# Kernel optimization log

Measured on AMD Instinct MI355X. Metric: run time of the kernel, lower is better.

## Reference

```python
import jax, jax.numpy as jnp
import numpy as np

RES0 = 128
SCALES = [1, 2, 4, 8]
OUT_DIM = 32
PLANES = [(0, 1), (0, 2), (1, 2)]  # itertools.combinations(range(3), 2)


def _bilinear(grid, cx, cy):
    """grid: [C,H,W]; cx maps to W, cy maps to H; coords in [-1,1].
    Matches F.grid_sample(mode='bilinear', align_corners=True, padding_mode='border')."""
    C, H, W = grid.shape
    x = jnp.clip((cx + 1.0) * 0.5 * (W - 1), 0.0, W - 1)
    y = jnp.clip((cy + 1.0) * 0.5 * (H - 1), 0.0, H - 1)
    x0 = jnp.floor(x)
    y0 = jnp.floor(y)
    wx = (x - x0)[:, None]  # [N,1]
    wy = (y - y0)[:, None]
    x0i = x0.astype(jnp.int32)
    y0i = y0.astype(jnp.int32)
    x1i = jnp.minimum(x0i + 1, W - 1)
    y1i = jnp.minimum(y0i + 1, H - 1)
    g00 = grid[:, y0i, x0i].T  # [N,C]
    g01 = grid[:, y0i, x1i].T
    g10 = grid[:, y1i, x0i].T
    g11 = grid[:, y1i, x1i].T
    top = g00 * (1.0 - wx) + g01 * wx
    bot = g10 * (1.0 - wx) + g11 * wx
    return top * (1.0 - wy) + bot * wy  # [N,C]


def _interpolate_ms_features(x, ms_grids):
    feats = []
    for scale_grids in ms_grids:  # fixed 4 scales
        interp_space = 1.0
        for ci, (a, b) in enumerate(PLANES):  # fixed 3 planes
            interp_space = interp_space * _bilinear(scale_grids[ci], x[:, a], x[:, b])
        feats.append(interp_space)
    return jnp.concatenate(feats, axis=-1)  # [N, 4*OUT_DIM]


def _mlp(f, w0, w1, w2):
    h = jax.nn.relu(f @ w0)
    h = jax.nn.relu(h @ w1)
    return h @ w2  # [N,1], linear output (tcnn, bias-free)


def setup_inputs() -> dict:
    key = jax.random.key(0)
    ks = jax.random.split(key, 16)
    N = 1_000_000
    inp = {"x": jax.random.uniform(ks[0], (N, 3), jnp.float32, -1.0, 1.0)}
    i = 1
    for s, mult in enumerate(SCALES):
        R = RES0 * mult
        for p in range(3):
            # nn.init.uniform_(a=0.1, b=0.5)
            inp[f"g{s}p{p}"] = jax.random.uniform(ks[i], (OUT_DIM, R, R), jnp.float32, 0.1, 0.5)
            i += 1
    F = OUT_DIM * len(SCALES)
    inp["w0"] = jax.random.normal(ks[13], (F, 64), jnp.float32) / np.sqrt(F).astype(np.float32)
    inp["w1"] = jax.random.normal(ks[14], (64, 64), jnp.float32) / 8.0
    inp["w2"] = jax.random.normal(ks[15], (64, 1), jnp.float32) / 8.0
    return inp


def reference(x, g0p0, g0p1, g0p2, g1p0, g1p1, g1p2, g2p0, g2p1, g2p2,
              g3p0, g3p1, g3p2, w0, w1, w2):
    ms_grids = [(g0p0, g0p1, g0p2), (g1p0, g1p1, g1p2),
                (g2p0, g2p1, g2p2), (g3p0, g3p1, g3p2)]
    features = _interpolate_ms_features(x, ms_grids)
    return _mlp(features, w0, w1, w2)
```

## Files before the change

### kernel.cpp

```cpp
#include <hip/hip_runtime.h>
#include <cstddef>


typedef unsigned short ushort_t;
typedef unsigned int uint_t;
typedef __bf16 bf16x8 __attribute__((ext_vector_type(8)));
typedef float f32x4 __attribute__((ext_vector_type(4)));

#define NBUCKET 32768

struct KParams {
  const float* x;
  const void* g[12];
  const float* w0;
  const float* w1;
  const float* w2;
  const ushort_t* w0T;
  const ushort_t* w1T;
  const float* xs;
  const int* sidx;
  float* out;
  int N;
};

struct TP3 {
  const float* src[3];
  ushort_t* dst[3];
  int RR;
};

__device__ __forceinline__ ushort_t f32_to_bf16_rne(float f) {
  uint_t u = __float_as_uint(f);
  u = (u + 0x7FFFu + ((u >> 16) & 1u)) >> 16;
  return (ushort_t)u;
}

__global__ __launch_bounds__(256) void transpose3(TP3 tp) {
  const float* __restrict__ in = tp.src[blockIdx.y];
  ushort_t* __restrict__ out = tp.dst[blockIdx.y];
  const int RR = tp.RR;
  __shared__ float tile[32][65];
  const int p0 = blockIdx.x * 64;
  {
    const int tp_ = threadIdx.x & 63;
    const int tc = threadIdx.x >> 6;
#pragma unroll
    for (int cc = 0; cc < 8; ++cc) {
      const int c = cc * 4 + tc;
      tile[c][tp_] = in[(size_t)c * RR + p0 + tp_];
    }
  }
  __syncthreads();
  {
    const int c2 = threadIdx.x & 15;
    const int tq = threadIdx.x >> 4;
    uint_t* o32 = (uint_t*)out;
#pragma unroll
    for (int pp = 0; pp < 4; ++pp) {
      const int pos = pp * 16 + tq;
      const uint_t lo = f32_to_bf16_rne(tile[2 * c2 + 0][pos]);
      const uint_t hi = f32_to_bf16_rne(tile[2 * c2 + 1][pos]);
      o32[(size_t)(p0 + pos) * 16 + c2] = lo | (hi << 16);
    }
  }
}

__global__ __launch_bounds__(256) void prep_weights(
    const float* __restrict__ w0, const float* __restrict__ w1,
    ushort_t* __restrict__ w0T, ushort_t* __restrict__ w1T) {
  const int t = threadIdx.x;
  for (int i = t; i < 128 * 64; i += 256) {
    const int k = i >> 6, n = i & 63;
    w0T[n * 128 + k] = f32_to_bf16_rne(w0[i]);
  }
  for (int i = t; i < 64 * 64; i += 256) {
    const int k = i >> 6, n = i & 63;
    w1T[n * 64 + k] = f32_to_bf16_rne(w1[i]);
  }
}

__device__ __forceinline__ uint_t spread5(uint_t v) {
  return (v & 1u) | ((v & 2u) << 2) | ((v & 4u) << 4) | ((v & 8u) << 6) |
         ((v & 16u) << 8);
}
__device__ __forceinline__ uint_t morton_key(const float* __restrict__ x,
                                             int i) {
  const float a = x[3 * i + 0];
  const float b = x[3 * i + 1];
  const float c = x[3 * i + 2];
  const uint_t ua = (uint_t)fminf(fmaxf((a + 1.0f) * 16.0f, 0.0f), 31.0f);
  const uint_t ub = (uint_t)fminf(fmaxf((b + 1.0f) * 16.0f, 0.0f), 31.0f);
  const uint_t uc = (uint_t)fminf(fmaxf((c + 1.0f) * 16.0f, 0.0f), 31.0f);
  return spread5(ua) | (spread5(ub) << 1) | (spread5(uc) << 2);
}

__global__ __launch_bounds__(256) void sort_hist(const float* __restrict__ x,
                                                 uint_t* __restrict__ cnt,
                                                 int N) {
  const int i = blockIdx.x * 256 + threadIdx.x;
  if (i < N) atomicAdd(&cnt[morton_key(x, i)], 1u);
}

__global__ __launch_bounds__(1024) void sort_scan(uint_t* __restrict__ cnt) {
  __shared__ uint_t s[1024];
  const int t = threadIdx.x;
  const int base = t * 32;
  uint_t p = 0;
#pragma unroll
  for (int e = 0; e < 32; ++e) p += cnt[base + e];
  s[t] = p;
  __syncthreads();
  for (int off = 1; off < 1024; off <<= 1) {
    uint_t v = 0;
    if (t >= off) v = s[t - off];
    __syncthreads();
    s[t] += v;
    __syncthreads();
  }
  uint_t running = s[t] - p;
#pragma unroll
  for (int e = 0; e < 32; ++e) {
    const uint_t old = cnt[base + e];
    cnt[base + e] = running;
    running += old;
  }
}

__global__ __launch_bounds__(256) void sort_scatter(
    const float* __restrict__ x, uint_t* __restrict__ cnt,
    int* __restrict__ sidx, float* __restrict__ xs, int N) {
  const int i = blockIdx.x * 256 + threadIdx.x;
  if (i >= N) return;
  const uint_t key = morton_key(x, i);
  const uint_t pos = atomicAdd(&cnt[key], 1u);
  sidx[pos] = i;
  xs[3 * pos + 0] = x[3 * i + 0];
  xs[3 * pos + 1] = x[3 * i + 1];
  xs[3 * pos + 2] = x[3 * i + 2];
}

template <bool SORTED>
__global__ __launch_bounds__(512, 8) void kplanes_fused_mfma(KParams P) {
  __shared__ float arena[10240];
  int* ci = (int*)arena;
  float* cf = arena;
  uint_t* feat32 = (uint_t*)(arena + 6144);
  float* px = arena + 6144;

  const int t = threadIdx.x;

  int bid = blockIdx.x;
  if (SORTED) {
    const int nblk = gridDim.x;
    const int q = nblk >> 3, r = nblk & 7;
    const int xcd = bid & 7, idx = bid >> 3;
    bid = (xcd < r ? xcd * (q + 1) : r * (q + 1) + (xcd - r) * q) + idx;
  }
  const int blk0 = bid * 64;

  if (SORTED) {
    if (t < 192) {
      int idx = blk0 * 3 + t;
      if (idx >= 3 * P.N) idx = 3 * P.N - 3 + (t % 3);
      px[t] = P.xs[idx];
    }
  } else {
    if (t < 192) {
      const int p = t / 3, e = t - p * 3;
      int Pi = blk0 + p;
      if (Pi >= P.N) Pi = P.N - 1;
      px[t] = P.x[3 * Pi + e];
    }
  }
  __syncthreads();

  for (int task = t; task < 768; task += 512) {
    const int pt = task & 63;
    const int sm = task >> 6;
    const int pl = sm >> 2;
    const int s = sm & 3;
    const float cx = (pl == 2) ? px[pt * 3 + 1] : px[pt * 3 + 0];
    const float cy = (pl == 0) ? px[pt * 3 + 1] : px[pt * 3 + 2];
    const int R = 128 << s;
    const float Rm1 = (float)(R - 1);
    const float u = fminf(fmaxf((cx + 1.0f) * 0.5f * Rm1, 0.0f), Rm1);
    const float v = fminf(fmaxf((cy + 1.0f) * 0.5f * Rm1, 0.0f), Rm1);
    const float fx0 = floorf(u), fy0 = floorf(v);
    const int x0 = (int)fx0, y0 = (int)fy0;
    const int x1 = min(x0 + 1, R - 1), y1 = min(y0 + 1, R - 1);
    const int base = task * 8;
    int4 o4;
    o4.x = y0 * R + x0;
    o4.y = y0 * R + x1;
    o4.z = y1 * R + x0;
    o4.w = y1 * R + x1;
    *(int4*)(ci + base) = o4;
    cf[base + 4] = u - fx0;
    cf[base + 5] = v - fy0;
  }
  __syncthreads();

  const int pt = t >> 3;
  const int q = t & 7;
  const int cg = q & 3;
  const int sh = q >> 2;
  uint_t* prow = feat32 + pt * 64;
  const int wxor = (pt & 7) << 2;

#pragma unroll
  for (int j = 0; j < 2; ++j) {
    const int s = 2 * j + sh;
    float f[8];
#pragma unroll
    for (int c = 0; c < 8; ++c) f[c] = 1.0f;

#pragma unroll
    for (int pl = 0; pl < 3; ++pl) {
      const int base = ((pl * 4 + s) * 64 + pt) * 8;
      const int4 o4 = *(const int4*)(ci + base);
      const float wx = cf[base + 4], wy = cf[base + 5];
      const float w11 = wx * wy;
      const float w10 = wy - w11;
      const float w01 = wx - w11;
      const float w00 = 1.0f - wx - w10;
      const ushort_t* gp = (const ushort_t*)P.g[s * 3 + pl];
      const uint4 qa = *(const uint4*)(gp + (size_t)o4.x * 32 + cg * 8);
      const uint4 qb = *(const uint4*)(gp + (size_t)o4.y * 32 + cg * 8);
      const uint4 qc = *(const uint4*)(gp + (size_t)o4.z * 32 + cg * 8);
      const uint4 qd = *(const uint4*)(gp + (size_t)o4.w * 32 + cg * 8);
#define CH2(dA, dB, dC, dD, i0, i1)                                \
  {                                                                \
    float rl = __uint_as_float((dD) << 16) * w11;                  \
    rl = fmaf(__uint_as_float((dC) << 16), w10, rl);               \
    rl = fmaf(__uint_as_float((dB) << 16), w01, rl);               \
    rl = fmaf(__uint_as_float((dA) << 16), w00, rl);               \
    f[i0] *= rl;                                                   \
    float rh = __uint_as_float((dD)&0xFFFF0000u) * w11;            \
    rh = fmaf(__uint_as_float((dC)&0xFFFF0000u), w10, rh);         \
    rh = fmaf(__uint_as_float((dB)&0xFFFF0000u), w01, rh);         \
    rh = fmaf(__uint_as_float((dA)&0xFFFF0000u), w00, rh);         \
    f[i1] *= rh;                                                   \
  }
      CH2(qa.x, qb.x, qc.x, qd.x, 0, 1)
      CH2(qa.y, qb.y, qc.y, qd.y, 2, 3)
      CH2(qa.z, qb.z, qc.z, qd.z, 4, 5)
      CH2(qa.w, qb.w, qc.w, qd.w, 6, 7)
#undef CH2
    }

    uint_t d0, d1, d2, d3;
    asm("v_cvt_pk_bf16_f32 %0, %1, %2" : "=v"(d0) : "v"(f[0]), "v"(f[1]));
    asm("v_cvt_pk_bf16_f32 %0, %1, %2" : "=v"(d1) : "v"(f[2]), "v"(f[3]));
    asm("v_cvt_pk_bf16_f32 %0, %1, %2" : "=v"(d2) : "v"(f[4]), "v"(f[5]));
    asm("v_cvt_pk_bf16_f32 %0, %1, %2" : "=v"(d3) : "v"(f[6]), "v"(f[7]));
    uint4 dv;
    dv.x = d0; dv.y = d1; dv.z = d2; dv.w = d3;
    *(uint4*)(prow + ((s * 16 + cg * 4) ^ wxor)) = dv;
  }
  __syncthreads();

  ushort_t* lds_h = (ushort_t*)arena;
  float(*oparts)[64] = (float(*)[64])(arena + 2048);

  const int w = __builtin_amdgcn_readfirstlane(t >> 6);
  const int mt = w & 3;
  const int nt0 = (w >> 2) << 1;
  const int ln = t & 15;
  const int lq = (t >> 4) & 3;
  const int arow = mt * 16 + ln;

  const uint_t* farow = feat32 + arow * 64;
  const int axor = (arow & 7) << 2;
  f32x4 acc0a = {0.f, 0.f, 0.f, 0.f}, acc0b = {0.f, 0.f, 0.f, 0.f};
  const ushort_t* w0a = P.w0T + (nt0 * 16 + ln) * 128 + lq * 8;
  const ushort_t* w0b = w0a + 16 * 128;
#pragma unroll
  for (int kt = 0; kt < 4; ++kt) {
    const bf16x8 aF = *(const bf16x8*)(farow + ((kt * 16 + lq * 4) ^ axor));
    const bf16x8 bFa = *(const bf16x8*)(w0a + kt * 32);
    const bf16x8 bFb = *(const bf16x8*)(w0b + kt * 32);
    acc0a = __builtin_amdgcn_mfma_f32_16x16x32_bf16(aF, bFa, acc0a, 0, 0, 0);
    acc0b = __builtin_amdgcn_mfma_f32_16x16x32_bf16(aF, bFb, acc0b, 0, 0, 0);
  }

#pragma unroll
  for (int i = 0; i < 2; ++i) {
    const f32x4 a = i ? acc0b : acc0a;
    const int col = (nt0 + i) * 16 + ln;
#pragma unroll
    for (int jj = 0; jj < 4; ++jj) {
      const float v = fmaxf(a[jj], 0.0f);
      uint_t dv;
      asm("v_cvt_pk_bf16_f32 %0, %1, %2" : "=v"(dv) : "v"(v), "v"(v));
      const int r = mt * 16 + lq * 4 + jj;
      lds_h[r * 64 + (col ^ ((r & 7) << 3))] = (ushort_t)dv;
    }
  }
  __syncthreads();

  const ushort_t* hrow = lds_h + arow * 64;
  const int hxor = (arow & 7) << 3;
  f32x4 acc1a = {0.f, 0.f, 0.f, 0.f}, acc1b = {0.f, 0.f, 0.f, 0.f};
  const ushort_t* w1a = P.w1T + (nt0 * 16 + ln) * 64 + lq * 8;
  const ushort_t* w1b = w1a + 16 * 64;
#pragma unroll
  for (int kt = 0; kt < 2; ++kt) {
    const bf16x8 aF = *(const bf16x8*)(hrow + ((kt * 32 + lq * 8) ^ hxor));
    const bf16x8 bFa = *(const bf16x8*)(w1a + kt * 32);
    const bf16x8 bFb = *(const bf16x8*)(w1b + kt * 32);
    acc1a = __builtin_amdgcn_mfma_f32_16x16x32_bf16(aF, bFa, acc1a, 0, 0, 0);
    acc1b = __builtin_amdgcn_mfma_f32_16x16x32_bf16(aF, bFb, acc1b, 0, 0, 0);
  }

  const float w2a = P.w2[nt0 * 16 + ln];
  const float w2b = P.w2[(nt0 + 1) * 16 + ln];
  float part[4];
#pragma unroll
  for (int jj = 0; jj < 4; ++jj)
    part[jj] = fmaxf(acc1a[jj], 0.f) * w2a + fmaxf(acc1b[jj], 0.f) * w2b;
#pragma unroll
  for (int jj = 0; jj < 4; ++jj) {
    part[jj] += __shfl_xor(part[jj], 1);
    part[jj] += __shfl_xor(part[jj], 2);
    part[jj] += __shfl_xor(part[jj], 4);
    part[jj] += __shfl_xor(part[jj], 8);
  }
  if (ln == 0) {
#pragma unroll
    for (int jj = 0; jj < 4; ++jj)
      oparts[w >> 2][mt * 16 + lq * 4 + jj] = part[jj];
  }
  __syncthreads();

  if (t < 64) {
    const int Po = blk0 + t;
    if (Po < P.N) {
      const float r = oparts[0][t] + oparts[1][t];
      if (SORTED)
        P.out[P.sidx[Po]] = r;
      else
        P.out[Po] = r;
    }
  }
}

__global__ __launch_bounds__(512, 8) void kplanes_fused_scalar(KParams P) {
  __shared__ float fl[64][130];
  const int t = threadIdx.x;
  const int pg = t >> 3;
  const int sub = t & 7;
  const int blk0 = blockIdx.x * 64;

  int Pi = blk0 + pg;
  if (Pi >= P.N) Pi = P.N - 1;
  const float c0 = P.x[3 * Pi + 0];
  const float c1 = P.x[3 * Pi + 1];
  const float c2 = P.x[3 * Pi + 2];

  float feat[4][4];
#pragma unroll
  for (int s = 0; s < 4; ++s)
#pragma unroll
    for (int c = 0; c < 4; ++c) feat[s][c] = 1.0f;

#pragma unroll
  for (int s = 0; s < 4; ++s) {
    const int R = 128 << s;
    const int RR = R * R;
#pragma unroll
    for (int pl = 0; pl < 3; ++pl) {
      const float cx = (pl == 2) ? c1 : c0;
      const float cy = (pl == 0) ? c1 : c2;
      const float Rm1 = (float)(R - 1);
      const float u = fminf(fmaxf((cx + 1.0f) * 0.5f * Rm1, 0.0f), Rm1);
      const float v = fminf(fmaxf((cy + 1.0f) * 0.5f * Rm1, 0.0f), Rm1);
      const float fx0 = floorf(u), fy0 = floorf(v);
      const float wx = u - fx0, wy = v - fy0;
      const int x0 = (int)fx0, y0 = (int)fy0;
      const int x1 = min(x0 + 1, R - 1), y1 = min(y0 + 1, R - 1);
      const float w11 = wx * wy;
      const float w10 = wy - w11;
      const float w01 = wx - w11;
      const float w00 = 1.0f - wx - w10;
      const float* gp = (const float*)P.g[s * 3 + pl];
      const int i00 = y0 * R + x0, i01 = y0 * R + x1;
      const int i10 = y1 * R + x0, i11 = y1 * R + x1;
#pragma unroll
      for (int c = 0; c < 4; ++c) {
        const size_t cb = (size_t)(sub * 4 + c) * RR;
        feat[s][c] *= gp[cb + i00] * w00 + gp[cb + i01] * w01 +
                      gp[cb + i10] * w10 + gp[cb + i11] * w11;
      }
    }
  }

#pragma unroll
  for (int s = 0; s < 4; ++s)
#pragma unroll
    for (int c = 0; c < 4; ++c)
      fl[pg][s * 32 + sub * 4 + c] = feat[s][c];
  __syncthreads();

  const int p = t & 63;
  const int g = __builtin_amdgcn_readfirstlane(t >> 6);

  const float* w0c = P.w0 + g * 8;
  float part[8];
#pragma unroll
  for (int jj = 0; jj < 8; ++jj) part[jj] = 0.0f;
#pragma unroll 16
  for (int k = 0; k < 128; ++k) {
    const float f = fl[p][k];
#pragma unroll
    for (int jj = 0; jj < 8; ++jj)
      part[jj] = fmaf(f, w0c[(size_t)k * 64 + jj], part[jj]);
  }
  __syncthreads();
#pragma unroll
  for (int jj = 0; jj < 8; ++jj)
    fl[p][g * 8 + jj] = fmaxf(part[jj], 0.0f);
  __syncthreads();

  const float* w1c = P.w1 + g * 8;
  float h1[8];
#pragma unroll
  for (int jj = 0; jj < 8; ++jj) h1[jj] = 0.0f;
#pragma unroll 16
  for (int k = 0; k < 64; ++k) {
    const float a = fl[p][k];
#pragma unroll
    for (int jj = 0; jj < 8; ++jj)
      h1[jj] = fmaf(a, w1c[(size_t)k * 64 + jj], h1[jj]);
  }

  const float* w2c = P.w2 + g * 8;
  float o = 0.0f;
#pragma unroll
  for (int jj = 0; jj < 8; ++jj)
    o = fmaf(fmaxf(h1[jj], 0.0f), w2c[jj], o);

  __syncthreads();
  ((float*)fl)[g * 64 + p] = o;
  __syncthreads();

  if (t < 64) {
    const int Po = blk0 + t;
    if (Po < P.N) {
      const float* f0 = (const float*)fl;
      float r = 0.0f;
#pragma unroll
      for (int j = 0; j < 8; ++j) r += f0[j * 64 + t];
      P.out[Po] = r;
    }
  }
}

extern "C" void kernel_launch(void* const* d_in, const int* in_sizes, int n_in,
                              void* d_out, int out_size, void* d_ws, size_t ws_size,
                              hipStream_t stream) {
  KParams P;
  P.x = (const float*)d_in[0];
  P.w0 = (const float*)d_in[13];
  P.w1 = (const float*)d_in[14];
  P.w2 = (const float*)d_in[15];
  P.out = (float*)d_out;
  const int N = in_sizes[0] / 3;
  P.N = N;
  P.xs = nullptr;
  P.sidx = nullptr;

  size_t need = 0;
  for (int s = 0; s < 4; ++s) {
    const size_t R = (size_t)(128 << s);
    need += 3ull * 32ull * R * R * sizeof(ushort_t);
  }
  const size_t walign = (need + 255) & ~(size_t)255;
  const size_t wbytes = (size_t)(64 * 128 + 64 * 64) * sizeof(ushort_t);
  const size_t cntoff = (walign + wbytes + 255) & ~(size_t)255;
  const size_t cntbytes = (size_t)NBUCKET * 4;
  const size_t sidxoff = cntoff + cntbytes;
  const size_t xsoff = (sidxoff + (size_t)N * 4 + 255) & ~(size_t)255;
  const size_t total_sorted = xsoff + (size_t)N * 12;

  const int nblk = (N + 63) / 64;
  if (ws_size >= walign + wbytes) {
    ushort_t* w = (ushort_t*)d_ws;
    size_t off = 0;
    for (int s = 0; s < 4; ++s) {
      const int R = 128 << s;
      const int RR = R * R;
      TP3 tp;
      tp.RR = RR;
      for (int pl = 0; pl < 3; ++pl) {
        tp.src[pl] = (const float*)d_in[1 + s * 3 + pl];
        tp.dst[pl] = w + off;
        P.g[s * 3 + pl] = w + off;
        off += (size_t)32 * RR;
      }
      dim3 grid(RR / 64, 3);
      transpose3<<<grid, 256, 0, stream>>>(tp);
    }
    ushort_t* w0T = (ushort_t*)((char*)d_ws + walign);
    ushort_t* w1T = w0T + 64 * 128;
    P.w0T = w0T;
    P.w1T = w1T;
    prep_weights<<<1, 256, 0, stream>>>(P.w0, P.w1, w0T, w1T);

    if (ws_size >= total_sorted) {
      uint_t* cnt = (uint_t*)((char*)d_ws + cntoff);
      int* sidx = (int*)((char*)d_ws + sidxoff);
      float* xs = (float*)((char*)d_ws + xsoff);
      hipMemsetAsync(cnt, 0, cntbytes, stream);
      const int pblk = (N + 255) / 256;
      sort_hist<<<pblk, 256, 0, stream>>>(P.x, cnt, N);
      sort_scan<<<1, 1024, 0, stream>>>(cnt);
      sort_scatter<<<pblk, 256, 0, stream>>>(P.x, cnt, sidx, xs, N);
      P.xs = xs;
      P.sidx = sidx;
      kplanes_fused_mfma<true><<<nblk, 512, 0, stream>>>(P);
    } else {
      kplanes_fused_mfma<false><<<nblk, 512, 0, stream>>>(P);
    }
  } else {
    for (int k = 0; k < 12; ++k) P.g[k] = (const void*)d_in[1 + k];
    P.w0T = nullptr;
    P.w1T = nullptr;
    kplanes_fused_scalar<<<nblk, 512, 0, stream>>>(P);
  }
}
```

Baseline: 656.6 us.

## Merge transposes into one launch, parallelize scan, pipeline plane gathers

```diff
diff --git a/kernel.cpp b/kernel.cpp
--- a/kernel.cpp
+++ b/kernel.cpp
@@ -23,10 +23,9 @@
   int N;
 };
 
-struct TP3 {
-  const float* src[3];
-  ushort_t* dst[3];
-  int RR;
+struct TPA {
+  const float* src[12];
+  ushort_t* dst[12];
 };
 
 __device__ __forceinline__ ushort_t f32_to_bf16_rne(float f) {
@@ -35,19 +34,27 @@
   return (ushort_t)u;
 }
 
-__global__ __launch_bounds__(256) void transpose3(TP3 tp) {
-  const float* __restrict__ in = tp.src[blockIdx.y];
-  ushort_t* __restrict__ out = tp.dst[blockIdx.y];
-  const int RR = tp.RR;
-  __shared__ float tile[32][65];
-  const int p0 = blockIdx.x * 64;
+__global__ __launch_bounds__(256) void transpose_all(TPA tp) {
+  const int b = blockIdx.x;
+  int s, tile;
+  if (b < 256) { s = 0; tile = b; }
+  else if (b < 1280) { s = 1; tile = b - 256; }
+  else if (b < 5376) { s = 2; tile = b - 1280; }
+  else { s = 3; tile = b - 5376; }
+  const int RR = 16384 << (2 * s);
+  const int k = s * 3 + blockIdx.y;
+  const float* __restrict__ in = tp.src[k];
+  ushort_t* __restrict__ out = tp.dst[k];
+
+  __shared__ float tile_s[32][65];
+  const int p0 = tile * 64;
   {
     const int tp_ = threadIdx.x & 63;
     const int tc = threadIdx.x >> 6;
 #pragma unroll
     for (int cc = 0; cc < 8; ++cc) {
       const int c = cc * 4 + tc;
-      tile[c][tp_] = in[(size_t)c * RR + p0 + tp_];
+      tile_s[c][tp_] = in[(size_t)c * RR + p0 + tp_];
     }
   }
   __syncthreads();
@@ -58,8 +65,8 @@
 #pragma unroll
     for (int pp = 0; pp < 4; ++pp) {
       const int pos = pp * 16 + tq;
-      const uint_t lo = f32_to_bf16_rne(tile[2 * c2 + 0][pos]);
-      const uint_t hi = f32_to_bf16_rne(tile[2 * c2 + 1][pos]);
+      const uint_t lo = f32_to_bf16_rne(tile_s[2 * c2 + 0][pos]);
+      const uint_t hi = f32_to_bf16_rne(tile_s[2 * c2 + 1][pos]);
       o32[(size_t)(p0 + pos) * 16 + c2] = lo | (hi << 16);
     }
   }
@@ -101,38 +108,57 @@
   if (i < N) atomicAdd(&cnt[morton_key(x, i)], 1u);
 }
 
-__global__ __launch_bounds__(1024) void sort_scan(uint_t* __restrict__ cnt) {
+__global__ __launch_bounds__(1024) void sort_scanA(uint_t* __restrict__ cnt,
+                                                   uint_t* __restrict__ bsum) {
   __shared__ uint_t s[1024];
   const int t = threadIdx.x;
-  const int base = t * 32;
-  uint_t p = 0;
-#pragma unroll
-  for (int e = 0; e < 32; ++e) p += cnt[base + e];
-  s[t] = p;
+  const int idx = blockIdx.x * 1024 + t;
+  const uint_t v = cnt[idx];
+  s[t] = v;
   __syncthreads();
   for (int off = 1; off < 1024; off <<= 1) {
-    uint_t v = 0;
-    if (t >= off) v = s[t - off];
+    uint_t u = 0;
+    if (t >= off) u = s[t - off];
     __syncthreads();
-    s[t] += v;
+    s[t] += u;
     __syncthreads();
   }
-  uint_t running = s[t] - p;
-#pragma unroll
-  for (int e = 0; e < 32; ++e) {
-    const uint_t old = cnt[base + e];
-    cnt[base + e] = running;
-    running += old;
+  cnt[idx] = s[t] - v;
+  if (t == 1023) bsum[blockIdx.x] = s[t];
+}
+
+__global__ __launch_bounds__(256) void sort_scanB_prepw(
+    uint_t* __restrict__ bsum, const float* __restrict__ w0,
+    const float* __restrict__ w1, ushort_t* __restrict__ w0T,
+    ushort_t* __restrict__ w1T) {
+  const int t = threadIdx.x;
+  if (t == 0) {
+    uint_t run = 0;
+#pragma unroll
+    for (int i = 0; i < 32; ++i) {
+      const uint_t c = bsum[i];
+      bsum[i] = run;
+      run += c;
+    }
+  }
+  for (int i = t; i < 128 * 64; i += 256) {
+    const int k = i >> 6, n = i & 63;
+    w0T[n * 128 + k] = f32_to_bf16_rne(w0[i]);
+  }
+  for (int i = t; i < 64 * 64; i += 256) {
+    const int k = i >> 6, n = i & 63;
+    w1T[n * 64 + k] = f32_to_bf16_rne(w1[i]);
   }
 }
 
 __global__ __launch_bounds__(256) void sort_scatter(
     const float* __restrict__ x, uint_t* __restrict__ cnt,
-    int* __restrict__ sidx, float* __restrict__ xs, int N) {
+    const uint_t* __restrict__ bsum, int* __restrict__ sidx,
+    float* __restrict__ xs, int N) {
   const int i = blockIdx.x * 256 + threadIdx.x;
   if (i >= N) return;
   const uint_t key = morton_key(x, i);
-  const uint_t pos = atomicAdd(&cnt[key], 1u);
+  const uint_t pos = atomicAdd(&cnt[key], 1u) + bsum[key >> 10];
   sidx[pos] = i;
   xs[3 * pos + 0] = x[3 * i + 0];
   xs[3 * pos + 1] = x[3 * i + 1];
@@ -141,11 +167,12 @@
 
 template <bool SORTED>
 __global__ __launch_bounds__(512, 8) void kplanes_fused_mfma(KParams P) {
-  __shared__ float arena[10240];
-  int* ci = (int*)arena;
-  float* cf = arena;
-  uint_t* feat32 = (uint_t*)(arena + 6144);
-  float* px = arena + 6144;
+  __shared__ float arena[8704];
+  int4* o4s = (int4*)arena;
+  float* wxs = arena + 3072;
+  float* wys = arena + 3840;
+  uint_t* feat32 = (uint_t*)(arena + 4608);
+  float* px = arena + 4608;
 
   const int t = threadIdx.x;
 
@@ -188,15 +215,14 @@
     const float fx0 = floorf(u), fy0 = floorf(v);
     const int x0 = (int)fx0, y0 = (int)fy0;
     const int x1 = min(x0 + 1, R - 1), y1 = min(y0 + 1, R - 1);
-    const int base = task * 8;
     int4 o4;
     o4.x = y0 * R + x0;
     o4.y = y0 * R + x1;
     o4.z = y1 * R + x0;
     o4.w = y1 * R + x1;
-    *(int4*)(ci + base) = o4;
-    cf[base + 4] = u - fx0;
-    cf[base + 5] = v - fy0;
+    o4s[task] = o4;
+    wxs[task] = u - fx0;
+    wys[task] = v - fy0;
   }
   __syncthreads();
 
@@ -207,27 +233,12 @@
   uint_t* prow = feat32 + pt * 64;
   const int wxor = (pt & 7) << 2;
 
-#pragma unroll
-  for (int j = 0; j < 2; ++j) {
-    const int s = 2 * j + sh;
-    float f[8];
-#pragma unroll
-    for (int c = 0; c < 8; ++c) f[c] = 1.0f;
-
-#pragma unroll
-    for (int pl = 0; pl < 3; ++pl) {
-      const int base = ((pl * 4 + s) * 64 + pt) * 8;
-      const int4 o4 = *(const int4*)(ci + base);
-      const float wx = cf[base + 4], wy = cf[base + 5];
-      const float w11 = wx * wy;
-      const float w10 = wy - w11;
-      const float w01 = wx - w11;
-      const float w00 = 1.0f - wx - w10;
-      const ushort_t* gp = (const ushort_t*)P.g[s * 3 + pl];
-      const uint4 qa = *(const uint4*)(gp + (size_t)o4.x * 32 + cg * 8);
-      const uint4 qb = *(const uint4*)(gp + (size_t)o4.y * 32 + cg * 8);
-      const uint4 qc = *(const uint4*)(gp + (size_t)o4.z * 32 + cg * 8);
-      const uint4 qd = *(const uint4*)(gp + (size_t)o4.w * 32 + cg * 8);
+#define LOADP(gp, o, QA, QB, QC, QD)                              \
+  QA = *(const uint4*)((gp) + (size_t)(o).x * 32 + cg * 8);       \
+  QB = *(const uint4*)((gp) + (size_t)(o).y * 32 + cg * 8);       \
+  QC = *(const uint4*)((gp) + (size_t)(o).z * 32 + cg * 8);       \
+  QD = *(const uint4*)((gp) + (size_t)(o).w * 32 + cg * 8);
+
 #define CH2(dA, dB, dC, dD, i0, i1)                                \
   {                                                                \
     float rl = __uint_as_float((dD) << 16) * w11;                  \
@@ -241,12 +252,43 @@
     rh = fmaf(__uint_as_float((dA)&0xFFFF0000u), w00, rh);         \
     f[i1] *= rh;                                                   \
   }
-      CH2(qa.x, qb.x, qc.x, qd.x, 0, 1)
-      CH2(qa.y, qb.y, qc.y, qd.y, 2, 3)
-      CH2(qa.z, qb.z, qc.z, qd.z, 4, 5)
-      CH2(qa.w, qb.w, qc.w, qd.w, 6, 7)
-#undef CH2
-    }
+
+#define CONSUME(QA, QB, QC, QD, WX, WY)                            \
+  {                                                                \
+    const float w11 = (WX) * (WY);                                 \
+    const float w10 = (WY)-w11;                                    \
+    const float w01 = (WX)-w11;                                    \
+    const float w00 = 1.0f - (WX)-w10;                             \
+    CH2(QA.x, QB.x, QC.x, QD.x, 0, 1)                              \
+    CH2(QA.y, QB.y, QC.y, QD.y, 2, 3)                              \
+    CH2(QA.z, QB.z, QC.z, QD.z, 4, 5)                              \
+    CH2(QA.w, QB.w, QC.w, QD.w, 6, 7)                              \
+  }
+
+#pragma unroll
+  for (int j = 0; j < 2; ++j) {
+    const int s = 2 * j + sh;
+    const int b0 = s * 64 + pt;
+    const int b1 = (4 + s) * 64 + pt;
+    const int b2 = (8 + s) * 64 + pt;
+    const int4 o0 = o4s[b0];
+    const int4 o1 = o4s[b1];
+    const int4 o2 = o4s[b2];
+    const float wx0 = wxs[b0], wy0 = wys[b0];
+    const float wx1 = wxs[b1], wy1 = wys[b1];
+    const float wx2 = wxs[b2], wy2 = wys[b2];
+    const ushort_t* g0 = (const ushort_t*)P.g[s * 3 + 0];
+    const ushort_t* g1 = (const ushort_t*)P.g[s * 3 + 1];
+    const ushort_t* g2 = (const ushort_t*)P.g[s * 3 + 2];
+
+    uint4 A0, B0, C0, D0, A1, B1, C1, D1, A2, B2, C2, D2;
+    LOADP(g0, o0, A0, B0, C0, D0)
+    LOADP(g1, o1, A1, B1, C1, D1)
+    float f[8] = {1.f, 1.f, 1.f, 1.f, 1.f, 1.f, 1.f, 1.f};
+    CONSUME(A0, B0, C0, D0, wx0, wy0)
+    LOADP(g2, o2, A2, B2, C2, D2)
+    CONSUME(A1, B1, C1, D1, wx1, wy1)
+    CONSUME(A2, B2, C2, D2, wx2, wy2)
 
     uint_t d0, d1, d2, d3;
     asm("v_cvt_pk_bf16_f32 %0, %1, %2" : "=v"(d0) : "v"(f[0]), "v"(f[1]));
@@ -257,6 +299,9 @@
     dv.x = d0; dv.y = d1; dv.z = d2; dv.w = d3;
     *(uint4*)(prow + ((s * 16 + cg * 4) ^ wxor)) = dv;
   }
+#undef LOADP
+#undef CH2
+#undef CONSUME
   __syncthreads();
 
   ushort_t* lds_h = (ushort_t*)arena;
@@ -478,47 +523,50 @@
   const size_t wbytes = (size_t)(64 * 128 + 64 * 64) * sizeof(ushort_t);
   const size_t cntoff = (walign + wbytes + 255) & ~(size_t)255;
   const size_t cntbytes = (size_t)NBUCKET * 4;
-  const size_t sidxoff = cntoff + cntbytes;
+  const size_t bsumoff = cntoff + cntbytes;
+  const size_t sidxoff = (bsumoff + 128 + 255) & ~(size_t)255;
   const size_t xsoff = (sidxoff + (size_t)N * 4 + 255) & ~(size_t)255;
   const size_t total_sorted = xsoff + (size_t)N * 12;
 
   const int nblk = (N + 63) / 64;
   if (ws_size >= walign + wbytes) {
     ushort_t* w = (ushort_t*)d_ws;
+    TPA tpa;
     size_t off = 0;
     for (int s = 0; s < 4; ++s) {
       const int R = 128 << s;
       const int RR = R * R;
-      TP3 tp;
-      tp.RR = RR;
       for (int pl = 0; pl < 3; ++pl) {
-        tp.src[pl] = (const float*)d_in[1 + s * 3 + pl];
-        tp.dst[pl] = w + off;
+        tpa.src[s * 3 + pl] = (const float*)d_in[1 + s * 3 + pl];
+        tpa.dst[s * 3 + pl] = w + off;
         P.g[s * 3 + pl] = w + off;
         off += (size_t)32 * RR;
       }
-      dim3 grid(RR / 64, 3);
-      transpose3<<<grid, 256, 0, stream>>>(tp);
-    }
+    }
+    dim3 tg(21760, 3);
+    transpose_all<<<tg, 256, 0, stream>>>(tpa);
+
     ushort_t* w0T = (ushort_t*)((char*)d_ws + walign);
     ushort_t* w1T = w0T + 64 * 128;
     P.w0T = w0T;
     P.w1T = w1T;
-    prep_weights<<<1, 256, 0, stream>>>(P.w0, P.w1, w0T, w1T);
 
     if (ws_size >= total_sorted) {
       uint_t* cnt = (uint_t*)((char*)d_ws + cntoff);
+      uint_t* bsum = (uint_t*)((char*)d_ws + bsumoff);
       int* sidx = (int*)((char*)d_ws + sidxoff);
       float* xs = (float*)((char*)d_ws + xsoff);
       hipMemsetAsync(cnt, 0, cntbytes, stream);
       const int pblk = (N + 255) / 256;
       sort_hist<<<pblk, 256, 0, stream>>>(P.x, cnt, N);
-      sort_scan<<<1, 1024, 0, stream>>>(cnt);
-      sort_scatter<<<pblk, 256, 0, stream>>>(P.x, cnt, sidx, xs, N);
+      sort_scanA<<<32, 1024, 0, stream>>>(cnt, bsum);
+      sort_scanB_prepw<<<1, 256, 0, stream>>>(bsum, P.w0, P.w1, w0T, w1T);
+      sort_scatter<<<pblk, 256, 0, stream>>>(P.x, cnt, bsum, sidx, xs, N);
       P.xs = xs;
       P.sidx = sidx;
       kplanes_fused_mfma<true><<<nblk, 512, 0, stream>>>(P);
     } else {
+      prep_weights<<<1, 256, 0, stream>>>(P.w0, P.w1, w0T, w1T);
       kplanes_fused_mfma<false><<<nblk, 512, 0, stream>>>(P);
     }
   } else {
```

New measurement: 713.8 us. 8.7% more time.
